# Kernel tuning notes

Measured on AMD Instinct MI355X. Metric: run time of the kernel, lower is better.

Reference implementation:

```python
import jax, jax.numpy as jnp
import numpy as np

N_UAV = 4096      # number of agents (rows/cols of adjacency)
T = 3             # filter_length (hard-coded to 3 in the module)
FEAT = 36         # 4 cameras x 9 xys features per UAV per step
N_VIS = 6         # n_vis_out
H = 256           # hidden width; layer_sizes = [18, 256, 256, 256, 2]
D_IN = T * N_VIS  # 18
D_OUT = 2


def _lin_init(key, fan_in, fan_out):
    # torch.nn.Linear default: U(-1/sqrt(fan_in), 1/sqrt(fan_in))
    b = 1.0 / np.sqrt(fan_in)
    kw, kb = jax.random.split(key)
    W = jax.random.uniform(kw, (fan_in, fan_out), jnp.float32, -b, b)
    bias = jax.random.uniform(kb, (fan_out,), jnp.float32, -b, b)
    return W, bias


def setup_inputs() -> dict:
    key = jax.random.key(0)
    ks = jax.random.split(key, 8)
    W_vis, b_vis = _lin_init(ks[2], FEAT, N_VIS)
    W_h0, b_h0 = _lin_init(ks[3], D_IN, H)
    W_h1, b_h1 = _lin_init(ks[4], H, H)
    W_h2, b_h2 = _lin_init(ks[5], H, H)
    W_p, b_p = _lin_init(ks[6], H, D_OUT)
    return {
        "vis_feats": jax.random.normal(ks[0], (N_UAV, T, FEAT), jnp.float32),
        "a_nets": jax.random.uniform(ks[1], (N_UAV, N_UAV, T), jnp.float32),
        "W_vis": W_vis, "b_vis": b_vis,
        "W_h0": W_h0, "b_h0": b_h0,
        "W_h1": W_h1, "b_h1": b_h1,
        "W_h2": W_h2, "b_h2": b_h2,
        "W_p": W_p, "b_p": b_p,
    }


def reference(vis_feats, a_nets, W_vis, b_vis, W_h0, b_h0, W_h1, b_h1,
              W_h2, b_h2, W_p, b_p):
    n = vis_feats.shape[0]
    n_vis = W_vis.shape[1]
    t_steps = a_nets.shape[2]
    x_agg = jnp.zeros((n, t_steps * n_vis), vis_feats.dtype)  # [N, 18]
    for t in range(t_steps):  # fixed small loop (filter_length = 3)
        a = a_nets[:, :, t]                       # [N, N]
        x = vis_feats[:, t, :] @ W_vis + b_vis    # vis_predict -> [N, 6]
        # x * a_net.unsqueeze(2) summed over dim 1 == a_net @ x
        msg = a @ x                               # [N, 6]
        # x_agg[:, :-6].unsqueeze(1).repeat(1,N,1) * a_net_comm summed over
        # dim 1 == x_agg[:, :-6] * rowsum(a_net)
        tail = x_agg[:, :-n_vis] * jnp.sum(a, axis=1, keepdims=True)  # [N, 12]
        x_agg = jnp.concatenate([msg, tail], axis=1)  # [N, 18]
    u = jax.nn.relu(x_agg @ W_h0 + b_h0)
    u = jax.nn.relu(u @ W_h1 + b_h1)
    u = jax.nn.relu(u @ W_h2 + b_h2)
    u = u @ W_p + b_p
    return (x_agg, u)
```

## Files before the change

### kernel.cpp

```cpp
#include <hip/hip_runtime.h>

#define N 4096
#define TSTEPS 3
#define FEAT 36
#define NVIS 6
#define HID 256
#define DIN 18
#define DOUT 2

#define JT 512

typedef __attribute__((ext_vector_type(8))) short bf16x8;
typedef __attribute__((ext_vector_type(4))) float f32x4;

__device__ __forceinline__ short f2bf(float f) {
    unsigned u = __builtin_bit_cast(unsigned, f);
    unsigned r = (u + 0x7FFFu + ((u >> 16) & 1u)) >> 16;
    return (short)r;
}

__device__ __forceinline__ int srow(int r) {
    return (r >> 5) * 672 + (r & 31) * 20 + ((r >> 2) & 7) * 4;
}

__global__ void k_prep(const float* __restrict__ vis, const float* __restrict__ Wv,
                       const float* __restrict__ bv, float* __restrict__ xall,
                       const float* __restrict__ W1, const float* __restrict__ W2,
                       short* __restrict__ Wp) {
    if (blockIdx.x < 288) {
        int o = blockIdx.x * 256 + threadIdx.x;
        if (o >= N * DIN) return;
        int j  = o / DIN;
        int ct = o - j * DIN;
        int t  = ct / NVIS;
        int c  = ct - t * NVIS;
        const float* vrow = vis + (size_t)j * (TSTEPS * FEAT) + t * FEAT;
        float acc = bv[c];
#pragma unroll
        for (int f = 0; f < FEAT; ++f) acc += vrow[f] * Wv[f * NVIS + c];
        xall[o] = acc;
    } else {
        int t = (blockIdx.x - 288) * 256 + threadIdx.x;
        int L  = t >> 16;
        int e  = t & 65535;
        int jj = e & 7;
        int l  = (e >> 3) & 63;
        int j  = (e >> 9) & 15;
        int s  = e >> 13;
        int k  = s * 32 + ((l >> 4) << 3) + jj;
        int n  = (j << 4) + (l & 15);
        const float* W = L ? W2 : W1;
        Wp[t] = f2bf(W[k * HID + n]);
    }
}

template<int FUSE>
__global__ void k_msg_mlp(const float* __restrict__ a, const float* __restrict__ xall,
                          float* __restrict__ xagg,
                          const short* __restrict__ Wp,
                          const float* __restrict__ W0, const float* __restrict__ b0,
                          const float* __restrict__ b1, const float* __restrict__ b2,
                          const float* __restrict__ Wpf, const float* __restrict__ bp,
                          float* __restrict__ u_out) {
    __shared__ union SM {
        float xs[16 * 672];
        struct {
            float xa[8][DIN];
            short hA[16 * 256];
            short hB[16 * 256];
            float h3[16 * 257];
        } m;
    } sm;
    const int tid  = threadIdx.x;
    const int lane = tid & 63;
    const int wave = tid >> 6;
    const int row0 = blockIdx.x * 8;
    const int row_base = row0 + wave * 2;

    const float* a0 = a + (size_t)row_base       * (N * 3);
    const float* a1 = a + (size_t)(row_base + 1) * (N * 3);

    float acc[2][3][6];
    float s[2][2];
#pragma unroll
    for (int r = 0; r < 2; ++r) {
#pragma unroll
        for (int t = 0; t < 3; ++t)
#pragma unroll
            for (int c = 0; c < 6; ++c) acc[r][t][c] = 0.f;
        s[r][0] = 0.f; s[r][1] = 0.f;
    }

    for (int tile = 0; tile < N / JT; ++tile) {
        const int tb = tile * JT;
        __syncthreads();
        for (int idx = tid; idx < JT * DIN; idx += 256) {
            int jj = idx / DIN;
            int c  = idx - jj * DIN;
            sm.xs[srow(jj) + c] = xall[(size_t)(tb + jj) * DIN + c];
        }
        __syncthreads();

#pragma unroll
        for (int chunk = 0; chunk < JT / 256; ++chunk) {
            const int jj = chunk * 256 + lane * 4;
            const size_t jb = (size_t)(tb + jj) * 3;
            const float4* pa0 = (const float4*)(a0 + jb);
            const float4* pa1 = (const float4*)(a1 + jb);
            float4 u0 = pa0[0], u1 = pa0[1], u2 = pa0[2];
            float4 v0 = pa1[0], v1 = pa1[1], v2 = pa1[2];
            const float av0[4][3] = {{u0.x,u0.y,u0.z},{u0.w,u1.x,u1.y},
                                     {u1.z,u1.w,u2.x},{u2.y,u2.z,u2.w}};
            const float av1[4][3] = {{v0.x,v0.y,v0.z},{v0.w,v1.x,v1.y},
                                     {v1.z,v1.w,v2.x},{v2.y,v2.z,v2.w}};
#pragma unroll
            for (int q = 0; q < 4; ++q) {
                const float* xr = sm.xs + srow(jj + q);
                float4 x0 = *(const float4*)(xr);
                float4 x1 = *(const float4*)(xr + 4);
                float4 x2 = *(const float4*)(xr + 8);
                float4 x3 = *(const float4*)(xr + 12);
                const float xv[18] = {x0.x,x0.y,x0.z,x0.w, x1.x,x1.y,x1.z,x1.w,
                                      x2.x,x2.y,x2.z,x2.w, x3.x,x3.y,x3.z,x3.w,
                                      xr[16], xr[17]};
#pragma unroll
                for (int t = 0; t < 3; ++t)
#pragma unroll
                    for (int c = 0; c < 6; ++c) {
                        acc[0][t][c] += av0[q][t] * xv[t*6+c];
                        acc[1][t][c] += av1[q][t] * xv[t*6+c];
                    }
                s[0][0] += av0[q][1]; s[0][1] += av0[q][2];
                s[1][0] += av1[q][1]; s[1][1] += av1[q][2];
            }
        }
    }

#pragma unroll
    for (int m = 1; m < 64; m <<= 1) {
#pragma unroll
        for (int r = 0; r < 2; ++r) {
#pragma unroll
            for (int t = 0; t < 3; ++t)
#pragma unroll
                for (int c = 0; c < 6; ++c)
                    acc[r][t][c] += __shfl_xor(acc[r][t][c], m, 64);
            s[r][0] += __shfl_xor(s[r][0], m, 64);
            s[r][1] += __shfl_xor(s[r][1], m, 64);
        }
    }

    __syncthreads();
    if (lane == 0) {
#pragma unroll
        for (int r = 0; r < 2; ++r) {
            const float s1 = s[r][0], s2 = s[r][1];
            float* xrow = sm.m.xa[wave * 2 + r];
#pragma unroll
            for (int c = 0; c < 6; ++c) {
                xrow[c]      = acc[r][2][c];
                xrow[6 + c]  = acc[r][1][c] * s2;
                xrow[12 + c] = acc[r][0][c] * s1 * s2;
            }
        }
    }
    __syncthreads();

    for (int idx = tid; idx < 8 * DIN; idx += 256) {
        int r = idx / DIN, e = idx - r * DIN;
        xagg[(size_t)(row0 + r) * DIN + e] = sm.m.xa[r][e];
    }

    if (!FUSE) return;

    {
        const int row = tid >> 5;
        const int n0  = (tid & 31) * 8;
        float accv[8];
#pragma unroll
        for (int jn = 0; jn < 8; ++jn) accv[jn] = b0[n0 + jn];
        for (int k = 0; k < DIN; ++k) {
            float4 wa = *(const float4*)&W0[k * HID + n0];
            float4 wb = *(const float4*)&W0[k * HID + n0 + 4];
            const float w[8] = {wa.x,wa.y,wa.z,wa.w, wb.x,wb.y,wb.z,wb.w};
            float xr = sm.m.xa[row][k];
#pragma unroll
            for (int jn = 0; jn < 8; ++jn) accv[jn] += xr * w[jn];
        }
        bf16x8 v;
#pragma unroll
        for (int jn = 0; jn < 8; ++jn) v[jn] = f2bf(fmaxf(accv[jn], 0.f));
        *(bf16x8*)&sm.m.hA[(row * 256 + n0) ^ ((row & 7) << 3)] = v;
    }
    __syncthreads();

    const int arow = lane & 15;
    const int kgrp = (lane >> 4) << 3;
    const int wv   = wave;
#pragma unroll 1
    for (int L = 0; L < 2; ++L) {
        const short* hsrc = L ? sm.m.hB : sm.m.hA;
        const float* bias = L ? b2 : b1;
        const short* WpL  = Wp + L * 65536;

        bf16x8 Af[8];
#pragma unroll
        for (int ks = 0; ks < 8; ++ks)
            Af[ks] = *(const bf16x8*)&hsrc[(arow * 256 + ks * 32 + kgrp) ^ ((arow & 7) << 3)];

        f32x4 c4[4];
#pragma unroll
        for (int jt = 0; jt < 4; ++jt) {
            float b = bias[wv * 64 + jt * 16 + (lane & 15)];
            c4[jt] = (f32x4){b, b, b, b};
        }
#pragma unroll
        for (int ks = 0; ks < 8; ++ks) {
#pragma unroll
            for (int jt = 0; jt < 4; ++jt) {
                int j = wv * 4 + jt;
                bf16x8 Bf = *(const bf16x8*)&WpL[(((ks * 16 + j) * 64) + lane) * 8];
                c4[jt] = __builtin_amdgcn_mfma_f32_16x16x32_bf16(Af[ks], Bf, c4[jt], 0, 0, 0);
            }
        }
#pragma unroll
        for (int jt = 0; jt < 4; ++jt) {
            int n = wv * 64 + jt * 16 + (lane & 15);
#pragma unroll
            for (int q = 0; q < 4; ++q) {
                int row = ((lane >> 4) << 2) + q;
                float v = fmaxf(c4[jt][q], 0.f);
                if (L == 0) sm.m.hB[(row * 256 + n) ^ ((row & 7) << 3)] = f2bf(v);
                else        sm.m.h3[row * 257 + n] = v;
            }
        }
        __syncthreads();
    }

    if (tid < 128) {
        const int r  = tid >> 4;
        const int d  = (tid >> 3) & 1;
        const int ks = tid & 7;
        float accf = 0.f;
        const float* hr = &sm.m.h3[r * 257 + ks * 32];
#pragma unroll
        for (int i = 0; i < 32; ++i) accf += hr[i] * Wpf[(ks * 32 + i) * DOUT + d];
        accf += __shfl_xor(accf, 1, 64);
        accf += __shfl_xor(accf, 2, 64);
        accf += __shfl_xor(accf, 4, 64);
        if (ks == 0) u_out[(size_t)(row0 + r) * DOUT + d] = accf + bp[d];
    }
}

#define HPITCH 20
__global__ __launch_bounds__(512, 2) void k_mlp(const float* __restrict__ xagg,
                      const float* __restrict__ W0, const float* __restrict__ b0,
                      const float* __restrict__ W1, const float* __restrict__ b1,
                      const float* __restrict__ W2, const float* __restrict__ b2,
                      const float* __restrict__ Wpf, const float* __restrict__ bp,
                      float* __restrict__ u_out) {
    __shared__ float xa[16][DIN];
    __shared__ float hb[2][HID][HPITCH];
    const int tid   = threadIdx.x;
    const int n     = tid & 255;
    const int rbase = (tid >> 8) * 8;
    const int base  = blockIdx.x * 16;

    for (int idx = tid; idx < 16 * DIN; idx += 512) {
        int r = idx / DIN, e = idx - r * DIN;
        xa[r][e] = xagg[(size_t)(base + r) * DIN + e];
    }
    __syncthreads();
    {
        float accv[8];
#pragma unroll
        for (int r = 0; r < 8; ++r) accv[r] = b0[n];
        for (int k = 0; k < DIN; ++k) {
            float w = W0[k * HID + n];
#pragma unroll
            for (int r = 0; r < 8; ++r) accv[r] += xa[rbase + r][k] * w;
        }
#pragma unroll
        for (int r = 0; r < 8; ++r) hb[0][n][rbase + r] = fmaxf(accv[r], 0.f);
    }
    __syncthreads();
    {
        float accv[8];
#pragma unroll
        for (int r = 0; r < 8; ++r) accv[r] = b1[n];
        for (int k = 0; k < HID; ++k) {
            float w = W1[k * HID + n];
            const float4* hp = (const float4*)&hb[0][k][rbase];
            float4 h0 = hp[0], h1 = hp[1];
            const float hv[8] = {h0.x,h0.y,h0.z,h0.w, h1.x,h1.y,h1.z,h1.w};
#pragma unroll
            for (int r = 0; r < 8; ++r) accv[r] += hv[r] * w;
        }
#pragma unroll
        for (int r = 0; r < 8; ++r) hb[1][n][rbase + r] = fmaxf(accv[r], 0.f);
    }
    __syncthreads();
    {
        float accv[8];
#pragma unroll
        for (int r = 0; r < 8; ++r) accv[r] = b2[n];
        for (int k = 0; k < HID; ++k) {
            float w = W2[k * HID + n];
            const float4* hp = (const float4*)&hb[1][k][rbase];
            float4 h0 = hp[0], h1 = hp[1];
            const float hv[8] = {h0.x,h0.y,h0.z,h0.w, h1.x,h1.y,h1.z,h1.w};
#pragma unroll
            for (int r = 0; r < 8; ++r) accv[r] += hv[r] * w;
        }
#pragma unroll
        for (int r = 0; r < 8; ++r) hb[0][n][rbase + r] = fmaxf(accv[r], 0.f);
    }
    __syncthreads();
    if (tid < 32) {
        int r = tid >> 1, d = tid & 1;
        float acc = bp[d];
        for (int k = 0; k < HID; ++k) acc += hb[0][k][r] * Wpf[k * DOUT + d];
        u_out[(size_t)(base + r) * DOUT + d] = acc;
    }
}

extern "C" void kernel_launch(void* const* d_in, const int* in_sizes, int n_in,
                              void* d_out, int out_size, void* d_ws, size_t ws_size,
                              hipStream_t stream) {
    const float* vis  = (const float*)d_in[0];
    const float* anet = (const float*)d_in[1];
    const float* Wv   = (const float*)d_in[2];
    const float* bv   = (const float*)d_in[3];
    const float* W0   = (const float*)d_in[4];
    const float* b0   = (const float*)d_in[5];
    const float* W1   = (const float*)d_in[6];
    const float* b1   = (const float*)d_in[7];
    const float* W2   = (const float*)d_in[8];
    const float* b2   = (const float*)d_in[9];
    const float* Wpf  = (const float*)d_in[10];
    const float* bp   = (const float*)d_in[11];

    float* xagg  = (float*)d_out;
    float* u_out = (float*)d_out + (size_t)N*DIN;
    float* xall  = (float*)d_ws;
    short* Wpk   = (short*)((char*)d_ws + (512 << 10));

    const bool fuse = ws_size >= (512 << 10) + 131072 * sizeof(short);

    if (fuse) {
        k_prep<<<800, 256, 0, stream>>>(vis, Wv, bv, xall, W1, W2, Wpk);
        k_msg_mlp<1><<<N / 8, 256, 0, stream>>>(anet, xall, xagg, Wpk,
                                                W0, b0, b1, b2, Wpf, bp, u_out);
    } else {
        k_prep<<<288, 256, 0, stream>>>(vis, Wv, bv, xall, W1, W2, Wpk);
        k_msg_mlp<0><<<N / 8, 256, 0, stream>>>(anet, xall, xagg, Wpk,
                                                W0, b0, b1, b2, Wpf, bp, u_out);
        k_mlp<<<N / 16, 512, 0, stream>>>(xagg, W0, b0, W1, b1, W2, b2, Wpf, bp, u_out);
    }
}
```

Before: 75.54 us.

## Read padded x rows straight from global memory and software-pipeline adjacency loads

The per-tile shared-memory staging of x (with its two barriers per tile) is replaced by direct global/L2 reads of xall, which is now written with a padded row pitch of 20 floats so rows can be read as aligned vector loads. The adjacency loop is double-buffered: the next chunk of a-values is loaded while the current one is computed. This removes the block-wide synchronisation and LDS traffic in the streaming phase, and it frees the large shared buffer, which may allow more blocks per CU. The cost is that every wave re-reads xall from cache instead of from LDS, so performance now depends on L1/L2 hit rates.

```diff
diff --git a/kernel.cpp b/kernel.cpp
--- a/kernel.cpp
+++ b/kernel.cpp
@@ -6,9 +6,8 @@
 #define NVIS 6
 #define HID 256
 #define DIN 18
+#define XP 20
 #define DOUT 2
-
-#define JT 512
 
 typedef __attribute__((ext_vector_type(8))) short bf16x8;
 typedef __attribute__((ext_vector_type(4))) float f32x4;
@@ -17,10 +16,6 @@
     unsigned u = __builtin_bit_cast(unsigned, f);
     unsigned r = (u + 0x7FFFu + ((u >> 16) & 1u)) >> 16;
     return (short)r;
-}
-
-__device__ __forceinline__ int srow(int r) {
-    return (r >> 5) * 672 + (r & 31) * 20 + ((r >> 2) & 7) * 4;
 }
 
 __global__ void k_prep(const float* __restrict__ vis, const float* __restrict__ Wv,
@@ -38,7 +33,7 @@
         float acc = bv[c];
 #pragma unroll
         for (int f = 0; f < FEAT; ++f) acc += vrow[f] * Wv[f * NVIS + c];
-        xall[o] = acc;
+        xall[(size_t)j * XP + ct] = acc;
     } else {
         int t = (blockIdx.x - 288) * 256 + threadIdx.x;
         int L  = t >> 16;
@@ -54,6 +49,50 @@
     }
 }
 
+struct AChunk { float4 u0, u1, u2, v0, v1, v2; };
+
+__device__ __forceinline__ AChunk aload(const float* __restrict__ a0,
+                                        const float* __restrict__ a1,
+                                        int lane, int ch) {
+    AChunk d;
+    const size_t jb = (size_t)(ch * 256 + lane * 4) * 3;
+    const float4* p0 = (const float4*)(a0 + jb);
+    const float4* p1 = (const float4*)(a1 + jb);
+    d.u0 = p0[0]; d.u1 = p0[1]; d.u2 = p0[2];
+    d.v0 = p1[0]; d.v1 = p1[1]; d.v2 = p1[2];
+    return d;
+}
+
+__device__ __forceinline__ void compute(const AChunk& d, const float* __restrict__ xall,
+                                        int lane, int ch,
+                                        float acc[2][3][6], float s[2][2]) {
+    const float av0[4][3] = {{d.u0.x,d.u0.y,d.u0.z},{d.u0.w,d.u1.x,d.u1.y},
+                             {d.u1.z,d.u1.w,d.u2.x},{d.u2.y,d.u2.z,d.u2.w}};
+    const float av1[4][3] = {{d.v0.x,d.v0.y,d.v0.z},{d.v0.w,d.v1.x,d.v1.y},
+                             {d.v1.z,d.v1.w,d.v2.x},{d.v2.y,d.v2.z,d.v2.w}};
+#pragma unroll
+    for (int q = 0; q < 4; ++q) {
+        const float* xr = xall + (size_t)(ch * 256 + lane * 4 + q) * XP;
+        float4 x0 = *(const float4*)(xr);
+        float4 x1 = *(const float4*)(xr + 4);
+        float4 x2 = *(const float4*)(xr + 8);
+        float4 x3 = *(const float4*)(xr + 12);
+        float2 x4 = *(const float2*)(xr + 16);
+        const float xv[18] = {x0.x,x0.y,x0.z,x0.w, x1.x,x1.y,x1.z,x1.w,
+                              x2.x,x2.y,x2.z,x2.w, x3.x,x3.y,x3.z,x3.w,
+                              x4.x,x4.y};
+#pragma unroll
+        for (int t = 0; t < 3; ++t)
+#pragma unroll
+            for (int c = 0; c < 6; ++c) {
+                acc[0][t][c] += av0[q][t] * xv[t*6+c];
+                acc[1][t][c] += av1[q][t] * xv[t*6+c];
+            }
+        s[0][0] += av0[q][1]; s[0][1] += av0[q][2];
+        s[1][0] += av1[q][1]; s[1][1] += av1[q][2];
+    }
+}
+
 template<int FUSE>
 __global__ void k_msg_mlp(const float* __restrict__ a, const float* __restrict__ xall,
                           float* __restrict__ xagg,
@@ -62,14 +101,11 @@
                           const float* __restrict__ b1, const float* __restrict__ b2,
                           const float* __restrict__ Wpf, const float* __restrict__ bp,
                           float* __restrict__ u_out) {
-    __shared__ union SM {
-        float xs[16 * 672];
-        struct {
-            float xa[8][DIN];
-            short hA[16 * 256];
-            short hB[16 * 256];
-            float h3[16 * 257];
-        } m;
+    __shared__ struct {
+        float xa[8][DIN];
+        short hA[16 * 256];
+        short hB[16 * 256];
+        float h3[16 * 257];
     } sm;
     const int tid  = threadIdx.x;
     const int lane = tid & 63;
@@ -91,48 +127,14 @@
         s[r][0] = 0.f; s[r][1] = 0.f;
     }
 
-    for (int tile = 0; tile < N / JT; ++tile) {
-        const int tb = tile * JT;
-        __syncthreads();
-        for (int idx = tid; idx < JT * DIN; idx += 256) {
-            int jj = idx / DIN;
-            int c  = idx - jj * DIN;
-            sm.xs[srow(jj) + c] = xall[(size_t)(tb + jj) * DIN + c];
-        }
-        __syncthreads();
-
-#pragma unroll
-        for (int chunk = 0; chunk < JT / 256; ++chunk) {
-            const int jj = chunk * 256 + lane * 4;
-            const size_t jb = (size_t)(tb + jj) * 3;
-            const float4* pa0 = (const float4*)(a0 + jb);
-            const float4* pa1 = (const float4*)(a1 + jb);
-            float4 u0 = pa0[0], u1 = pa0[1], u2 = pa0[2];
-            float4 v0 = pa1[0], v1 = pa1[1], v2 = pa1[2];
-            const float av0[4][3] = {{u0.x,u0.y,u0.z},{u0.w,u1.x,u1.y},
-                                     {u1.z,u1.w,u2.x},{u2.y,u2.z,u2.w}};
-            const float av1[4][3] = {{v0.x,v0.y,v0.z},{v0.w,v1.x,v1.y},
-                                     {v1.z,v1.w,v2.x},{v2.y,v2.z,v2.w}};
-#pragma unroll
-            for (int q = 0; q < 4; ++q) {
-                const float* xr = sm.xs + srow(jj + q);
-                float4 x0 = *(const float4*)(xr);
-                float4 x1 = *(const float4*)(xr + 4);
-                float4 x2 = *(const float4*)(xr + 8);
-                float4 x3 = *(const float4*)(xr + 12);
-                const float xv[18] = {x0.x,x0.y,x0.z,x0.w, x1.x,x1.y,x1.z,x1.w,
-                                      x2.x,x2.y,x2.z,x2.w, x3.x,x3.y,x3.z,x3.w,
-                                      xr[16], xr[17]};
-#pragma unroll
-                for (int t = 0; t < 3; ++t)
-#pragma unroll
-                    for (int c = 0; c < 6; ++c) {
-                        acc[0][t][c] += av0[q][t] * xv[t*6+c];
-                        acc[1][t][c] += av1[q][t] * xv[t*6+c];
-                    }
-                s[0][0] += av0[q][1]; s[0][1] += av0[q][2];
-                s[1][0] += av1[q][1]; s[1][1] += av1[q][2];
-            }
+    {
+        AChunk A = aload(a0, a1, lane, 0);
+#pragma unroll
+        for (int ch = 0; ch < 16; ch += 2) {
+            AChunk B = aload(a0, a1, lane, ch + 1);
+            compute(A, xall, lane, ch, acc, s);
+            if (ch + 2 < 16) A = aload(a0, a1, lane, ch + 2);
+            compute(B, xall, lane, ch + 1, acc, s);
         }
     }
 
@@ -150,12 +152,11 @@
         }
     }
 
-    __syncthreads();
     if (lane == 0) {
 #pragma unroll
         for (int r = 0; r < 2; ++r) {
             const float s1 = s[r][0], s2 = s[r][1];
-            float* xrow = sm.m.xa[wave * 2 + r];
+            float* xrow = sm.xa[wave * 2 + r];
 #pragma unroll
             for (int c = 0; c < 6; ++c) {
                 xrow[c]      = acc[r][2][c];
@@ -168,7 +169,7 @@
 
     for (int idx = tid; idx < 8 * DIN; idx += 256) {
         int r = idx / DIN, e = idx - r * DIN;
-        xagg[(size_t)(row0 + r) * DIN + e] = sm.m.xa[r][e];
+        xagg[(size_t)(row0 + r) * DIN + e] = sm.xa[r][e];
     }
 
     if (!FUSE) return;
@@ -183,14 +184,14 @@
             float4 wa = *(const float4*)&W0[k * HID + n0];
             float4 wb = *(const float4*)&W0[k * HID + n0 + 4];
             const float w[8] = {wa.x,wa.y,wa.z,wa.w, wb.x,wb.y,wb.z,wb.w};
-            float xr = sm.m.xa[row][k];
+            float xr = sm.xa[row][k];
 #pragma unroll
             for (int jn = 0; jn < 8; ++jn) accv[jn] += xr * w[jn];
         }
         bf16x8 v;
 #pragma unroll
         for (int jn = 0; jn < 8; ++jn) v[jn] = f2bf(fmaxf(accv[jn], 0.f));
-        *(bf16x8*)&sm.m.hA[(row * 256 + n0) ^ ((row & 7) << 3)] = v;
+        *(bf16x8*)&sm.hA[(row * 256 + n0) ^ ((row & 7) << 3)] = v;
     }
     __syncthreads();
 
@@ -199,7 +200,7 @@
     const int wv   = wave;
 #pragma unroll 1
     for (int L = 0; L < 2; ++L) {
-        const short* hsrc = L ? sm.m.hB : sm.m.hA;
+        const short* hsrc = L ? sm.hB : sm.hA;
         const float* bias = L ? b2 : b1;
         const short* WpL  = Wp + L * 65536;
 
@@ -230,8 +231,8 @@
             for (int q = 0; q < 4; ++q) {
                 int row = ((lane >> 4) << 2) + q;
                 float v = fmaxf(c4[jt][q], 0.f);
-                if (L == 0) sm.m.hB[(row * 256 + n) ^ ((row & 7) << 3)] = f2bf(v);
-                else        sm.m.h3[row * 257 + n] = v;
+                if (L == 0) sm.hB[(row * 256 + n) ^ ((row & 7) << 3)] = f2bf(v);
+                else        sm.h3[row * 257 + n] = v;
             }
         }
         __syncthreads();
@@ -242,7 +243,7 @@
         const int d  = (tid >> 3) & 1;
         const int ks = tid & 7;
         float accf = 0.f;
-        const float* hr = &sm.m.h3[r * 257 + ks * 32];
+        const float* hr = &sm.h3[r * 257 + ks * 32];
 #pragma unroll
         for (int i = 0; i < 32; ++i) accf += hr[i] * Wpf[(ks * 32 + i) * DOUT + d];
         accf += __shfl_xor(accf, 1, 64);
```

Measured after the change: 109.2 us. 1.45x slower.

## Transpose vis projections, stage larger smem tiles, and prefetch adjacency chunks three ahead

Applied to the files above, without the earlier changes.

The precomputed vis projections are now stored column-major (feature by agent), so the message kernel can stage 2048-agent tiles into shared memory with contiguous float4 copies and read them as float4 per feature. The streaming loads of the adjacency rows are software-pipelined with a three-deep register prefetch, so global loads overlap the FMA work. Launch bounds are set to one block per SM, and there are fewer shared-memory staging syncs. In exchange, register use and shared-memory footprint grow (a 144KB tile), which may limit occupancy.

```diff
diff --git a/kernel.cpp b/kernel.cpp
--- a/kernel.cpp
+++ b/kernel.cpp
@@ -7,8 +7,7 @@
 #define HID 256
 #define DIN 18
 #define DOUT 2
-
-#define JT 512
+#define HT 2048
 
 typedef __attribute__((ext_vector_type(8))) short bf16x8;
 typedef __attribute__((ext_vector_type(4))) float f32x4;
@@ -19,26 +18,21 @@
     return (short)r;
 }
 
-__device__ __forceinline__ int srow(int r) {
-    return (r >> 5) * 672 + (r & 31) * 20 + ((r >> 2) & 7) * 4;
-}
-
 __global__ void k_prep(const float* __restrict__ vis, const float* __restrict__ Wv,
-                       const float* __restrict__ bv, float* __restrict__ xall,
+                       const float* __restrict__ bv, float* __restrict__ xallT,
                        const float* __restrict__ W1, const float* __restrict__ W2,
                        short* __restrict__ Wp) {
     if (blockIdx.x < 288) {
         int o = blockIdx.x * 256 + threadIdx.x;
-        if (o >= N * DIN) return;
-        int j  = o / DIN;
-        int ct = o - j * DIN;
-        int t  = ct / NVIS;
-        int c  = ct - t * NVIS;
+        int c = o >> 12;
+        int j = o & 4095;
+        int t  = c / NVIS;
+        int cc = c - t * NVIS;
         const float* vrow = vis + (size_t)j * (TSTEPS * FEAT) + t * FEAT;
-        float acc = bv[c];
-#pragma unroll
-        for (int f = 0; f < FEAT; ++f) acc += vrow[f] * Wv[f * NVIS + c];
-        xall[o] = acc;
+        float acc = bv[cc];
+#pragma unroll
+        for (int f = 0; f < FEAT; ++f) acc += vrow[f] * Wv[f * NVIS + cc];
+        xallT[(size_t)c * N + j] = acc;
     } else {
         int t = (blockIdx.x - 288) * 256 + threadIdx.x;
         int L  = t >> 16;
@@ -54,16 +48,31 @@
     }
 }
 
+struct AChunk { float4 u0, u1, u2, v0, v1, v2; };
+
+__device__ __forceinline__ AChunk aload(const float* __restrict__ a0,
+                                        const float* __restrict__ a1,
+                                        int lane, int g) {
+    AChunk d;
+    const size_t jb = (size_t)(g * 256 + lane * 4) * 3;
+    const float4* p0 = (const float4*)(a0 + jb);
+    const float4* p1 = (const float4*)(a1 + jb);
+    d.u0 = p0[0]; d.u1 = p0[1]; d.u2 = p0[2];
+    d.v0 = p1[0]; d.v1 = p1[1]; d.v2 = p1[2];
+    return d;
+}
+
 template<int FUSE>
-__global__ void k_msg_mlp(const float* __restrict__ a, const float* __restrict__ xall,
-                          float* __restrict__ xagg,
-                          const short* __restrict__ Wp,
-                          const float* __restrict__ W0, const float* __restrict__ b0,
-                          const float* __restrict__ b1, const float* __restrict__ b2,
-                          const float* __restrict__ Wpf, const float* __restrict__ bp,
-                          float* __restrict__ u_out) {
-    __shared__ union SM {
-        float xs[16 * 672];
+__global__ __launch_bounds__(256, 1)
+void k_msg_mlp(const float* __restrict__ a, const float* __restrict__ xallT,
+               float* __restrict__ xagg,
+               const short* __restrict__ Wp,
+               const float* __restrict__ W0, const float* __restrict__ b0,
+               const float* __restrict__ b1, const float* __restrict__ b2,
+               const float* __restrict__ Wpf, const float* __restrict__ bp,
+               float* __restrict__ u_out) {
+    __shared__ union {
+        float xT[DIN][HT];
         struct {
             float xa[8][DIN];
             short hA[16 * 256];
@@ -91,48 +100,49 @@
         s[r][0] = 0.f; s[r][1] = 0.f;
     }
 
-    for (int tile = 0; tile < N / JT; ++tile) {
-        const int tb = tile * JT;
-        __syncthreads();
-        for (int idx = tid; idx < JT * DIN; idx += 256) {
-            int jj = idx / DIN;
-            int c  = idx - jj * DIN;
-            sm.xs[srow(jj) + c] = xall[(size_t)(tb + jj) * DIN + c];
-        }
-        __syncthreads();
-
-#pragma unroll
-        for (int chunk = 0; chunk < JT / 256; ++chunk) {
-            const int jj = chunk * 256 + lane * 4;
-            const size_t jb = (size_t)(tb + jj) * 3;
-            const float4* pa0 = (const float4*)(a0 + jb);
-            const float4* pa1 = (const float4*)(a1 + jb);
-            float4 u0 = pa0[0], u1 = pa0[1], u2 = pa0[2];
-            float4 v0 = pa1[0], v1 = pa1[1], v2 = pa1[2];
-            const float av0[4][3] = {{u0.x,u0.y,u0.z},{u0.w,u1.x,u1.y},
-                                     {u1.z,u1.w,u2.x},{u2.y,u2.z,u2.w}};
-            const float av1[4][3] = {{v0.x,v0.y,v0.z},{v0.w,v1.x,v1.y},
-                                     {v1.z,v1.w,v2.x},{v2.y,v2.z,v2.w}};
-#pragma unroll
-            for (int q = 0; q < 4; ++q) {
-                const float* xr = sm.xs + srow(jj + q);
-                float4 x0 = *(const float4*)(xr);
-                float4 x1 = *(const float4*)(xr + 4);
-                float4 x2 = *(const float4*)(xr + 8);
-                float4 x3 = *(const float4*)(xr + 12);
-                const float xv[18] = {x0.x,x0.y,x0.z,x0.w, x1.x,x1.y,x1.z,x1.w,
-                                      x2.x,x2.y,x2.z,x2.w, x3.x,x3.y,x3.z,x3.w,
-                                      xr[16], xr[17]};
-#pragma unroll
-                for (int t = 0; t < 3; ++t)
-#pragma unroll
-                    for (int c = 0; c < 6; ++c) {
-                        acc[0][t][c] += av0[q][t] * xv[t*6+c];
-                        acc[1][t][c] += av1[q][t] * xv[t*6+c];
-                    }
-                s[0][0] += av0[q][1]; s[0][1] += av0[q][2];
-                s[1][0] += av1[q][1]; s[1][1] += av1[q][2];
-            }
+    AChunk p0 = aload(a0, a1, lane, 0);
+    AChunk p1 = aload(a0, a1, lane, 1);
+    AChunk p2 = aload(a0, a1, lane, 2);
+
+#pragma unroll
+    for (int g = 0; g < 16; ++g) {
+        if ((g & 7) == 0) {
+            const int tile = g >> 3;
+            __syncthreads();
+#pragma unroll
+            for (int k = 0; k < 36; ++k) {
+                int idx = tid + k * 256;
+                int c   = idx >> 9;
+                int off = (idx & 511) << 2;
+                *(float4*)&sm.xT[c][off] =
+                    *(const float4*)&xallT[(size_t)c * N + tile * HT + off];
+            }
+            __syncthreads();
+        }
+        AChunk cur = p0; p0 = p1; p1 = p2;
+        if (g + 3 < 16) p2 = aload(a0, a1, lane, g + 3);
+
+        const float av0[4][3] = {{cur.u0.x,cur.u0.y,cur.u0.z},{cur.u0.w,cur.u1.x,cur.u1.y},
+                                 {cur.u1.z,cur.u1.w,cur.u2.x},{cur.u2.y,cur.u2.z,cur.u2.w}};
+        const float av1[4][3] = {{cur.v0.x,cur.v0.y,cur.v0.z},{cur.v0.w,cur.v1.x,cur.v1.y},
+                                 {cur.v1.z,cur.v1.w,cur.v2.x},{cur.v2.y,cur.v2.z,cur.v2.w}};
+        const int jb = (g & 7) * 256 + lane * 4;
+#pragma unroll
+        for (int t = 0; t < 3; ++t)
+#pragma unroll
+            for (int c = 0; c < 6; ++c) {
+                float4 xv = *(const float4*)&sm.xT[t * 6 + c][jb];
+                const float xq[4] = {xv.x, xv.y, xv.z, xv.w};
+#pragma unroll
+                for (int q = 0; q < 4; ++q) {
+                    acc[0][t][c] += av0[q][t] * xq[q];
+                    acc[1][t][c] += av1[q][t] * xq[q];
+                }
+            }
+#pragma unroll
+        for (int q = 0; q < 4; ++q) {
+            s[0][0] += av0[q][1]; s[0][1] += av0[q][2];
+            s[1][0] += av1[q][1]; s[1][1] += av1[q][2];
         }
     }
 
@@ -342,18 +352,18 @@
 
     float* xagg  = (float*)d_out;
     float* u_out = (float*)d_out + (size_t)N*DIN;
-    float* xall  = (float*)d_ws;
+    float* xallT = (float*)d_ws;
     short* Wpk   = (short*)((char*)d_ws + (512 << 10));
 
     const bool fuse = ws_size >= (512 << 10) + 131072 * sizeof(short);
 
     if (fuse) {
-        k_prep<<<800, 256, 0, stream>>>(vis, Wv, bv, xall, W1, W2, Wpk);
-        k_msg_mlp<1><<<N / 8, 256, 0, stream>>>(anet, xall, xagg, Wpk,
+        k_prep<<<800, 256, 0, stream>>>(vis, Wv, bv, xallT, W1, W2, Wpk);
+        k_msg_mlp<1><<<N / 8, 256, 0, stream>>>(anet, xallT, xagg, Wpk,
                                                 W0, b0, b1, b2, Wpf, bp, u_out);
     } else {
-        k_prep<<<288, 256, 0, stream>>>(vis, Wv, bv, xall, W1, W2, Wpk);
-        k_msg_mlp<0><<<N / 8, 256, 0, stream>>>(anet, xall, xagg, Wpk,
+        k_prep<<<288, 256, 0, stream>>>(vis, Wv, bv, xallT, W1, W2, Wpk);
+        k_msg_mlp<0><<<N / 8, 256, 0, stream>>>(anet, xallT, xagg, Wpk,
                                                 W0, b0, b1, b2, Wpf, bp, u_out);
         k_mlp<<<N / 16, 512, 0, stream>>>(xagg, W0, b0, W1, b1, W2, b2, Wpf, bp, u_out);
     }
```

New measurement: 113.4 us. 1.5x slower.
